# Kernel tuning notes

Measured on AMD Instinct MI355X. Metric: run time of the kernel, lower is better.

The kernel has to match this reference:

```python
import jax, jax.numpy as jnp
import numpy as np

N = 100000
E = 1600000
F_IN = 128
HID = 64
N_CLS = 16


def gcn_conv(x, row, col, W, b, n_nodes):
    # x: [N, Fin]; row/col: [E+N] (self-loops already appended)
    h = x @ W  # [N, Fout]
    ones = jnp.ones(row.shape[0], dtype=x.dtype)
    deg = jax.ops.segment_sum(ones, col, num_segments=n_nodes)  # in-degree incl. self-loop
    dinv = jnp.where(deg > 0, jax.lax.rsqrt(deg), 0.0)
    norm = dinv[row] * dinv[col]  # [E+N]
    msg = h[row] * norm[:, None]  # gather + scale
    out = jax.ops.segment_sum(msg, col, num_segments=n_nodes)  # scatter-add
    return out + b


def setup_inputs() -> dict:
    key = jax.random.key(0)
    k1, k2, k3, k4, k5, k6 = jax.random.split(key, 6)
    x = jax.random.normal(k1, (N, F_IN), dtype=jnp.float32)
    edge_index = jax.random.randint(k2, (2, E), 0, N, dtype=jnp.int64)
    # Glorot-ish init for weights
    W1 = jax.random.normal(k3, (F_IN, HID), dtype=jnp.float32) / np.sqrt(F_IN)
    b1 = jnp.zeros((HID,), dtype=jnp.float32)
    W2 = jax.random.normal(k4, (HID, N_CLS), dtype=jnp.float32) / np.sqrt(HID)
    b2 = jnp.zeros((N_CLS,), dtype=jnp.float32)
    return {"x": x, "edge_index": edge_index, "W1": W1, "b1": b1, "W2": W2, "b2": b2}


def reference(x, edge_index, W1, b1, W2, b2):
    # Add self-loops (GCNConv default add_self_loops=True)
    loop = jnp.arange(N, dtype=edge_index.dtype)
    row = jnp.concatenate([edge_index[0], loop])
    col = jnp.concatenate([edge_index[1], loop])
    h = gcn_conv(x, row, col, W1, b1, N)
    h = jax.nn.relu(h)
    h = gcn_conv(h, row, col, W2, b2, N)
    return jax.nn.log_softmax(h, axis=1)
```

## Files before the change

kernel.cpp:

```cpp
#include <hip/hip_runtime.h>
#include <hip/hip_fp16.h>

#define F_IN 128
#define HID  64
#define NCLS 16
#define NPB  128
#define CAP  4096
#define CHUNK 16384
#define W1PAD 136
#define CSTRIDE 4

typedef _Float16 half_t;
typedef __attribute__((ext_vector_type(8))) _Float16 half8;
typedef __attribute__((ext_vector_type(4))) float float4v;


__global__ __launch_bounds__(256) void bin_gemm(
    const int* __restrict__ row, const int* __restrict__ col,
    const float* __restrict__ x, const float* __restrict__ W1,
    int* __restrict__ cursor, int* __restrict__ ebuf,
    __half* __restrict__ hs1, int N, int E, int NB, int nbin)
{
    __shared__ __align__(16) char smem[17408];
    int t = threadIdx.x;

    if ((int)blockIdx.x < nbin) {
        int* hist = (int*)smem;
        int* base = (int*)smem + 1024;
        int* off  = (int*)smem + 2048;
        for (int i = t; i < NB; i += 256) hist[i] = 0;
        int base_e = blockIdx.x * CHUNK;
        __syncthreads();
        #pragma unroll 4
        for (int s = 0; s < 16; ++s) {
            int ej = base_e + s * 1024 + t * 4;
            int nv = min(max(E - ej, 0), 4);
            if (nv == 4) {
                int4 c4 = *(const int4*)&col[ej];
                atomicAdd(&hist[c4.x >> 7], 1);
                atomicAdd(&hist[c4.y >> 7], 1);
                atomicAdd(&hist[c4.z >> 7], 1);
                atomicAdd(&hist[c4.w >> 7], 1);
            } else {
                for (int q = ej; q < E; ++q) atomicAdd(&hist[col[q] >> 7], 1);
            }
        }
        __syncthreads();
        for (int i = t; i < NB; i += 256) {
            int h = hist[i];
            base[i] = h ? (i * CAP + atomicAdd(&cursor[i * CSTRIDE], h)) : 0;
            off[i] = 0;
        }
        __syncthreads();
        #pragma unroll 4
        for (int s = 0; s < 16; ++s) {
            int ej = base_e + s * 1024 + t * 4;
            int nv = min(max(E - ej, 0), 4);
            if (nv == 4) {
                int4 c4 = *(const int4*)&col[ej];
                int4 r4 = *(const int4*)&row[ej];
                int b0 = c4.x >> 7; int p0 = base[b0] + atomicAdd(&off[b0], 1);
                if (p0 < (b0 + 1) * CAP) ebuf[p0] = (r4.x << 7) | (c4.x & (NPB - 1));
                int b1 = c4.y >> 7; int p1 = base[b1] + atomicAdd(&off[b1], 1);
                if (p1 < (b1 + 1) * CAP) ebuf[p1] = (r4.y << 7) | (c4.y & (NPB - 1));
                int b2 = c4.z >> 7; int p2 = base[b2] + atomicAdd(&off[b2], 1);
                if (p2 < (b2 + 1) * CAP) ebuf[p2] = (r4.z << 7) | (c4.z & (NPB - 1));
                int b3 = c4.w >> 7; int p3 = base[b3] + atomicAdd(&off[b3], 1);
                if (p3 < (b3 + 1) * CAP) ebuf[p3] = (r4.w << 7) | (c4.w & (NPB - 1));
            } else {
                for (int q = ej; q < E; ++q) {
                    int c = col[q], b = c >> 7;
                    int p = base[b] + atomicAdd(&off[b], 1);
                    if (p < (b + 1) * CAP) ebuf[p] = (row[q] << 7) | (c & (NPB - 1));
                }
            }
        }
        return;
    }

    half_t* W1l = (half_t*)smem;
    for (int i = t; i < F_IN * HID; i += 256) {
        int k = i >> 6, n = i & 63;
        W1l[n * W1PAD + k] = (half_t)W1[i];
    }
    __syncthreads();

    int b = blockIdx.x - nbin;
    int node0 = b << 7;
    int wv = t >> 6, lane = t & 63;
    int l15 = lane & 15, quad = lane >> 4;
    int mbase = wv * 32;
    int r0 = min(node0 + mbase + l15, N - 1);
    int r1 = min(node0 + mbase + 16 + l15, N - 1);
    const float* x0 = x + (size_t)r0 * F_IN;
    const float* x1 = x + (size_t)r1 * F_IN;
    float4v acc[2][4];
    #pragma unroll
    for (int mt = 0; mt < 2; ++mt)
        #pragma unroll
        for (int j = 0; j < 4; ++j) acc[mt][j] = (float4v){0.f, 0.f, 0.f, 0.f};
    #pragma unroll
    for (int kb = 0; kb < 4; ++kb) {
        int off = kb * 32 + quad * 8;
        float4 fa = *(const float4*)&x0[off];
        float4 fb = *(const float4*)&x0[off + 4];
        float4 ga = *(const float4*)&x1[off];
        float4 gb = *(const float4*)&x1[off + 4];
        half8 a0 = {(half_t)fa.x, (half_t)fa.y, (half_t)fa.z, (half_t)fa.w,
                    (half_t)fb.x, (half_t)fb.y, (half_t)fb.z, (half_t)fb.w};
        half8 a1 = {(half_t)ga.x, (half_t)ga.y, (half_t)ga.z, (half_t)ga.w,
                    (half_t)gb.x, (half_t)gb.y, (half_t)gb.z, (half_t)gb.w};
        #pragma unroll
        for (int j = 0; j < 4; ++j) {
            half8 bv = *(const half8*)&W1l[(j * 16 + l15) * W1PAD + off];
            acc[0][j] = __builtin_amdgcn_mfma_f32_16x16x32_f16(a0, bv, acc[0][j], 0, 0, 0);
            acc[1][j] = __builtin_amdgcn_mfma_f32_16x16x32_f16(a1, bv, acc[1][j], 0, 0, 0);
        }
    }
    #pragma unroll
    for (int mt = 0; mt < 2; ++mt)
        #pragma unroll
        for (int j = 0; j < 4; ++j)
            #pragma unroll
            for (int r = 0; r < 4; ++r) {
                int m = mbase + mt * 16 + quad * 4 + r;
                int nn = node0 + m;
                if (nn < N) hs1[(size_t)nn * HID + j * 16 + l15] =
                    __float2half(acc[mt][j][r]);
            }
}


__global__ __launch_bounds__(256) void csr_scale(
    const int* __restrict__ ebuf, const int* __restrict__ cursor,
    int2* __restrict__ rsc, int* __restrict__ csr_row,
    __half* __restrict__ hs1, int N)
{
    __shared__ int hist[NPB];
    __shared__ float dv[NPB];
    __shared__ int cur[NPB];
    __shared__ int wtot;
    int t = threadIdx.x;
    int b = blockIdx.x;
    int node0 = b << 7;
    int ebase = b * CAP;

    int p[8];
    #pragma unroll
    for (int k = 0; k < 8; ++k) p[k] = ebuf[ebase + t + 256 * k];
    int cnt = min(cursor[b * CSTRIDE], CAP);
    if (t < NPB) hist[t] = 0;
    __syncthreads();
    #pragma unroll
    for (int k = 0; k < 8; ++k)
        if (t + 256 * k < cnt) atomicAdd(&hist[p[k] & (NPB - 1)], 1);
    if (cnt > 2048)
        for (int e = 2048 + t; e < cnt; e += 256)
            atomicAdd(&hist[ebuf[ebase + e] & (NPB - 1)], 1);
    __syncthreads();

    int h = 0, incl = 0;
    if (t < NPB) {
        h = hist[t];
        incl = h;
        #pragma unroll
        for (int off = 1; off < 64; off <<= 1) {
            int u = __shfl_up(incl, off, 64);
            if ((t & 63) >= off) incl += u;
        }
        if (t == 63) wtot = incl;
        dv[t] = rsqrtf((float)h + 1.0f);
    }
    __syncthreads();
    if (t < NPB) {
        if (t >= 64) incl += wtot;
        int start = ebase + incl - h;
        cur[t] = start;
        int n = node0 + t;
        if (n < N) rsc[n] = make_int2(start, h);
    }
    __syncthreads();

    #pragma unroll
    for (int k = 0; k < 8; ++k)
        if (t + 256 * k < cnt) {
            int pos = atomicAdd(&cur[p[k] & (NPB - 1)], 1);
            csr_row[pos] = p[k] >> 7;
        }
    if (cnt > 2048)
        for (int e = 2048 + t; e < cnt; e += 256) {
            int pp = ebuf[ebase + e];
            int pos = atomicAdd(&cur[pp & (NPB - 1)], 1);
            csr_row[pos] = pp >> 7;
        }

    half8* H = (half8*)hs1;
    for (int i = t; i < 1024; i += 256) {
        int r = i >> 3, s8 = i & 7;
        int n = node0 + r;
        if (n < N) {
            half8 v = H[(size_t)n * 8 + s8];
            float d = dv[r];
            #pragma unroll
            for (int k = 0; k < 8; ++k) v[k] = (half_t)((float)v[k] * d);
            H[(size_t)n * 8 + s8] = v;
        }
    }
}


__global__ __launch_bounds__(256) void agg_l1(
    const __half* __restrict__ hs1, const int2* __restrict__ rsc,
    const int* __restrict__ csr, const float* __restrict__ b1,
    const float* __restrict__ W2, __half* __restrict__ h2s, int N)
{
    __shared__ float W2l[HID * NCLS];
    __shared__ float o1[32][65];
    for (int i = threadIdx.x; i < HID * NCLS; i += 256) W2l[i] = W2[i];
    __syncthreads();
    int w = threadIdx.x >> 6, lane = threadIdx.x & 63;
    int g = lane >> 3, gl = lane & 7;
    int rowi = w * 8 + g;
    int c = blockIdx.x * 32 + rowi;
    bool active = (c < N);
    int cc = active ? c : 0;
    int2 rc = rsc[cc];
    int e0 = rc.x, e1 = rc.x + rc.y;
    float dc = rsqrtf((float)rc.y + 1.0f);
    const half8* H = (const half8*)hs1;
    half8 sv = H[(size_t)cc * 8 + gl];
    float sum[8];
    #pragma unroll
    for (int k = 0; k < 8; ++k) sum[k] = (float)sv[k];
    int i = e0;
    for (; i + 8 <= e1; i += 8) {
        int id[8];
        #pragma unroll
        for (int s = 0; s < 8; ++s) id[s] = csr[i + s];
        half8 a[8];
        #pragma unroll
        for (int s = 0; s < 8; ++s) a[s] = H[(size_t)id[s] * 8 + gl];
        half8 t0 = a[0] + a[1];
        half8 t1 = a[2] + a[3];
        half8 t2 = a[4] + a[5];
        half8 t3 = a[6] + a[7];
        half8 v = (t0 + t1) + (t2 + t3);
        #pragma unroll
        for (int k = 0; k < 8; ++k) sum[k] += (float)v[k];
    }
    if (i < e1) {
        int e1m1 = e1 - 1;
        int id[8];
        #pragma unroll
        for (int s = 0; s < 8; ++s) id[s] = csr[min(i + s, e1m1)];
        half8 a[8];
        #pragma unroll
        for (int s = 0; s < 8; ++s) a[s] = H[(size_t)id[s] * 8 + gl];
        #pragma unroll
        for (int s = 0; s < 8; ++s) {
            float fm = (i + s < e1) ? 1.f : 0.f;
            #pragma unroll
            for (int k = 0; k < 8; ++k) sum[k] = fmaf(fm, (float)a[s][k], sum[k]);
        }
    }
    float4 bb0 = *(const float4*)&b1[gl * 8];
    float4 bb1 = *(const float4*)&b1[gl * 8 + 4];
    o1[rowi][gl * 8 + 0] = fmaxf(fmaf(dc, sum[0], bb0.x), 0.f);
    o1[rowi][gl * 8 + 1] = fmaxf(fmaf(dc, sum[1], bb0.y), 0.f);
    o1[rowi][gl * 8 + 2] = fmaxf(fmaf(dc, sum[2], bb0.z), 0.f);
    o1[rowi][gl * 8 + 3] = fmaxf(fmaf(dc, sum[3], bb0.w), 0.f);
    o1[rowi][gl * 8 + 4] = fmaxf(fmaf(dc, sum[4], bb1.x), 0.f);
    o1[rowi][gl * 8 + 5] = fmaxf(fmaf(dc, sum[5], bb1.y), 0.f);
    o1[rowi][gl * 8 + 6] = fmaxf(fmaf(dc, sum[6], bb1.z), 0.f);
    o1[rowi][gl * 8 + 7] = fmaxf(fmaf(dc, sum[7], bb1.w), 0.f);
    int j0 = gl * 2, j1 = gl * 2 + 1;
    float s0 = 0.f, s1 = 0.f;
    const float* orow = o1[rowi];
    #pragma unroll 8
    for (int k = 0; k < HID; ++k) {
        float ov = orow[k];
        s0 = fmaf(ov, W2l[k * NCLS + j0], s0);
        s1 = fmaf(ov, W2l[k * NCLS + j1], s1);
    }
    if (active) {
        __half2 hv;
        hv.x = __float2half(dc * s0);
        hv.y = __float2half(dc * s1);
        ((__half2*)h2s)[(size_t)c * 8 + gl] = hv;
    }
}


__global__ __launch_bounds__(256) void agg2_final(
    const __half* __restrict__ h2s, const int2* __restrict__ rsc,
    const int* __restrict__ csr, const float* __restrict__ b2,
    float* __restrict__ out, int N)
{
    int t = threadIdx.x;
    int w = t >> 6, lane = t & 63;
    int nw = lane >> 1, hl = lane & 1;
    int c = blockIdx.x * 128 + w * 32 + nw;
    bool active = (c < N);
    int cc = active ? c : 0;
    int2 rc = rsc[cc];
    int e0 = rc.x, e1 = rc.x + rc.y;
    float dcv = rsqrtf((float)rc.y + 1.0f);
    const half8* H = (const half8*)h2s;
    half8 sv = H[(size_t)cc * 2 + hl];
    float sum[8];
    #pragma unroll
    for (int k = 0; k < 8; ++k) sum[k] = (float)sv[k];
    int i = e0;
    for (; i + 8 <= e1; i += 8) {
        int id[8];
        #pragma unroll
        for (int s = 0; s < 8; ++s) id[s] = csr[i + s];
        half8 a[8];
        #pragma unroll
        for (int s = 0; s < 8; ++s) a[s] = H[(size_t)id[s] * 2 + hl];
        half8 t0 = a[0] + a[1];
        half8 t1 = a[2] + a[3];
        half8 t2 = a[4] + a[5];
        half8 t3 = a[6] + a[7];
        half8 v = (t0 + t1) + (t2 + t3);
        #pragma unroll
        for (int k = 0; k < 8; ++k) sum[k] += (float)v[k];
    }
    if (i < e1) {
        int e1m1 = e1 - 1;
        int id[8];
        #pragma unroll
        for (int s = 0; s < 8; ++s) id[s] = csr[min(i + s, e1m1)];
        half8 a[8];
        #pragma unroll
        for (int s = 0; s < 8; ++s) a[s] = H[(size_t)id[s] * 2 + hl];
        #pragma unroll
        for (int s = 0; s < 8; ++s) {
            float fm = (i + s < e1) ? 1.f : 0.f;
            #pragma unroll
            for (int k = 0; k < 8; ++k) sum[k] = fmaf(fm, (float)a[s][k], sum[k]);
        }
    }
    float4 bb0 = *(const float4*)&b2[hl * 8];
    float4 bb1 = *(const float4*)&b2[hl * 8 + 4];
    float v0 = fmaf(dcv, sum[0], bb0.x);
    float v1 = fmaf(dcv, sum[1], bb0.y);
    float v2 = fmaf(dcv, sum[2], bb0.z);
    float v3 = fmaf(dcv, sum[3], bb0.w);
    float v4 = fmaf(dcv, sum[4], bb1.x);
    float v5 = fmaf(dcv, sum[5], bb1.y);
    float v6 = fmaf(dcv, sum[6], bb1.z);
    float v7 = fmaf(dcv, sum[7], bb1.w);
    float mx = fmaxf(fmaxf(fmaxf(v0, v1), fmaxf(v2, v3)),
                     fmaxf(fmaxf(v4, v5), fmaxf(v6, v7)));
    mx = fmaxf(mx, __shfl_xor(mx, 1, 64));
    float s = __expf(v0 - mx) + __expf(v1 - mx) + __expf(v2 - mx) + __expf(v3 - mx)
            + __expf(v4 - mx) + __expf(v5 - mx) + __expf(v6 - mx) + __expf(v7 - mx);
    s += __shfl_xor(s, 1, 64);
    float lse = mx + __logf(s);
    if (active) {
        float* o = out + (size_t)c * NCLS + hl * 8;
        *(float4*)&o[0] = make_float4(v0 - lse, v1 - lse, v2 - lse, v3 - lse);
        *(float4*)&o[4] = make_float4(v4 - lse, v5 - lse, v6 - lse, v7 - lse);
    }
}


extern "C" void kernel_launch(void* const* d_in, const int* in_sizes, int n_in,
                              void* d_out, int out_size, void* d_ws, size_t ws_size,
                              hipStream_t stream) {
    const float* x  = (const float*)d_in[0];
    const int*   ei = (const int*)d_in[1];
    const float* W1 = (const float*)d_in[2];
    const float* b1 = (const float*)d_in[3];
    const float* W2 = (const float*)d_in[4];
    const float* b2 = (const float*)d_in[5];
    float* out = (float*)d_out;

    const int N = in_sizes[0] / F_IN;
    const int E = in_sizes[1] / 2;
    const int* row = ei;
    const int* col = ei + E;

    const int NB = (N + NPB - 1) / NPB;
    size_t Np  = ((size_t)N + 15) & ~(size_t)15;
    size_t NBp = ((size_t)NB + 15) & ~(size_t)15;
    size_t Rg  = (size_t)NB * CAP;

    char* p = (char*)d_ws;
    __half* hs1     = (__half*)p;  p += Np * HID * 2;
    __half* h2s     = (__half*)p;  p += Np * NCLS * 2;
    int2*   rsc     = (int2*)p;    p += Np * 8;
    int*    csr_row = (int*)p;     p += Rg * 4;
    int*    ebuf    = (int*)p;     p += Rg * 4;
    int*    cursor  = (int*)p;     p += NBp * 4 * CSTRIDE;

    int nbin = (E + CHUNK - 1) / CHUNK;

    hipMemsetAsync(cursor, 0, NBp * sizeof(int) * CSTRIDE, stream);
    bin_gemm<<<nbin + NB, 256, 0, stream>>>(row, col, x, W1, cursor, ebuf,
                                            hs1, N, E, NB, nbin);
    csr_scale<<<NB, 256, 0, stream>>>(ebuf, cursor, rsc, csr_row, hs1, N);
    agg_l1<<<(N + 31) / 32, 256, 0, stream>>>(hs1, rsc, csr_row, b1, W2, h2s, N);
    agg2_final<<<(N + 127) / 128, 256, 0, stream>>>(h2s, rsc, csr_row, b2, out, N);
}
```

Measured before the change: 184.7 us.

## Split GEMM from binning and fuse dinv scaling into GEMM epilogue

The layer-1 GEMM moves out of the binning kernel into its own launch that runs after the CSR/degree kernel. This lets it multiply by dinv directly in the epilogue, which removes the separate read-modify-write pass over hs1 in csr_scale. Output goes through an LDS staging tile so rows are written as coalesced half8 stores. The W1 transpose is now done once into global memory and read from there instead of per-block LDS. The cost is one extra kernel launch and losing the overlap between binning and GEMM.

```diff
diff --git a/kernel.cpp b/kernel.cpp
--- a/kernel.cpp
+++ b/kernel.cpp
@@ -7,86 +7,161 @@
 #define NPB  128
 #define CAP  4096
 #define CHUNK 16384
-#define W1PAD 136
 #define CSTRIDE 4
+#define SPAD 72
 
 typedef _Float16 half_t;
 typedef __attribute__((ext_vector_type(8))) _Float16 half8;
 typedef __attribute__((ext_vector_type(4))) float float4v;
 
 
-__global__ __launch_bounds__(256) void bin_gemm(
+__global__ __launch_bounds__(256) void bin_w1(
     const int* __restrict__ row, const int* __restrict__ col,
-    const float* __restrict__ x, const float* __restrict__ W1,
-    int* __restrict__ cursor, int* __restrict__ ebuf,
-    __half* __restrict__ hs1, int N, int E, int NB, int nbin)
+    const float* __restrict__ W1, int* __restrict__ cursor,
+    int* __restrict__ ebuf, half_t* __restrict__ W1t,
+    int E, int NB, int nbin)
 {
-    __shared__ __align__(16) char smem[17408];
+    __shared__ int hist[1024], base[1024], off[1024];
     int t = threadIdx.x;
 
-    if ((int)blockIdx.x < nbin) {
-        int* hist = (int*)smem;
-        int* base = (int*)smem + 1024;
-        int* off  = (int*)smem + 2048;
-        for (int i = t; i < NB; i += 256) hist[i] = 0;
-        int base_e = blockIdx.x * CHUNK;
-        __syncthreads();
-        #pragma unroll 4
-        for (int s = 0; s < 16; ++s) {
-            int ej = base_e + s * 1024 + t * 4;
-            int nv = min(max(E - ej, 0), 4);
-            if (nv == 4) {
-                int4 c4 = *(const int4*)&col[ej];
-                atomicAdd(&hist[c4.x >> 7], 1);
-                atomicAdd(&hist[c4.y >> 7], 1);
-                atomicAdd(&hist[c4.z >> 7], 1);
-                atomicAdd(&hist[c4.w >> 7], 1);
-            } else {
-                for (int q = ej; q < E; ++q) atomicAdd(&hist[col[q] >> 7], 1);
+    if ((int)blockIdx.x >= nbin) {
+        for (int i = t; i < F_IN * HID; i += 256) {
+            int k = i >> 6, n = i & 63;
+            W1t[n * F_IN + k] = (half_t)W1[i];
+        }
+        return;
+    }
+    for (int i = t; i < NB; i += 256) hist[i] = 0;
+    int base_e = blockIdx.x * CHUNK;
+    __syncthreads();
+    #pragma unroll 4
+    for (int s = 0; s < 16; ++s) {
+        int ej = base_e + s * 1024 + t * 4;
+        int nv = min(max(E - ej, 0), 4);
+        if (nv == 4) {
+            int4 c4 = *(const int4*)&col[ej];
+            atomicAdd(&hist[c4.x >> 7], 1);
+            atomicAdd(&hist[c4.y >> 7], 1);
+            atomicAdd(&hist[c4.z >> 7], 1);
+            atomicAdd(&hist[c4.w >> 7], 1);
+        } else {
+            for (int q = ej; q < E; ++q) atomicAdd(&hist[col[q] >> 7], 1);
+        }
+    }
+    __syncthreads();
+    for (int i = t; i < NB; i += 256) {
+        int h = hist[i];
+        base[i] = h ? (i * CAP + atomicAdd(&cursor[i * CSTRIDE], h)) : 0;
+        off[i] = 0;
+    }
+    __syncthreads();
+    #pragma unroll 4
+    for (int s = 0; s < 16; ++s) {
+        int ej = base_e + s * 1024 + t * 4;
+        int nv = min(max(E - ej, 0), 4);
+        if (nv == 4) {
+            int4 c4 = *(const int4*)&col[ej];
+            int4 r4 = *(const int4*)&row[ej];
+            int b0 = c4.x >> 7; int p0 = base[b0] + atomicAdd(&off[b0], 1);
+            if (p0 < (b0 + 1) * CAP) ebuf[p0] = (r4.x << 7) | (c4.x & (NPB - 1));
+            int b1 = c4.y >> 7; int p1 = base[b1] + atomicAdd(&off[b1], 1);
+            if (p1 < (b1 + 1) * CAP) ebuf[p1] = (r4.y << 7) | (c4.y & (NPB - 1));
+            int b2 = c4.z >> 7; int p2 = base[b2] + atomicAdd(&off[b2], 1);
+            if (p2 < (b2 + 1) * CAP) ebuf[p2] = (r4.z << 7) | (c4.z & (NPB - 1));
+            int b3 = c4.w >> 7; int p3 = base[b3] + atomicAdd(&off[b3], 1);
+            if (p3 < (b3 + 1) * CAP) ebuf[p3] = (r4.w << 7) | (c4.w & (NPB - 1));
+        } else {
+            for (int q = ej; q < E; ++q) {
+                int c = col[q], b = c >> 7;
+                int p = base[b] + atomicAdd(&off[b], 1);
+                if (p < (b + 1) * CAP) ebuf[p] = (row[q] << 7) | (c & (NPB - 1));
             }
         }
-        __syncthreads();
-        for (int i = t; i < NB; i += 256) {
-            int h = hist[i];
-            base[i] = h ? (i * CAP + atomicAdd(&cursor[i * CSTRIDE], h)) : 0;
-            off[i] = 0;
-        }
-        __syncthreads();
-        #pragma unroll 4
-        for (int s = 0; s < 16; ++s) {
-            int ej = base_e + s * 1024 + t * 4;
-            int nv = min(max(E - ej, 0), 4);
-            if (nv == 4) {
-                int4 c4 = *(const int4*)&col[ej];
-                int4 r4 = *(const int4*)&row[ej];
-                int b0 = c4.x >> 7; int p0 = base[b0] + atomicAdd(&off[b0], 1);
-                if (p0 < (b0 + 1) * CAP) ebuf[p0] = (r4.x << 7) | (c4.x & (NPB - 1));
-                int b1 = c4.y >> 7; int p1 = base[b1] + atomicAdd(&off[b1], 1);
-                if (p1 < (b1 + 1) * CAP) ebuf[p1] = (r4.y << 7) | (c4.y & (NPB - 1));
-                int b2 = c4.z >> 7; int p2 = base[b2] + atomicAdd(&off[b2], 1);
-                if (p2 < (b2 + 1) * CAP) ebuf[p2] = (r4.z << 7) | (c4.z & (NPB - 1));
-                int b3 = c4.w >> 7; int p3 = base[b3] + atomicAdd(&off[b3], 1);
-                if (p3 < (b3 + 1) * CAP) ebuf[p3] = (r4.w << 7) | (c4.w & (NPB - 1));
-            } else {
-                for (int q = ej; q < E; ++q) {
-                    int c = col[q], b = c >> 7;
-                    int p = base[b] + atomicAdd(&off[b], 1);
-                    if (p < (b + 1) * CAP) ebuf[p] = (row[q] << 7) | (c & (NPB - 1));
-                }
-            }
-        }
-        return;
-    }
-
-    half_t* W1l = (half_t*)smem;
-    for (int i = t; i < F_IN * HID; i += 256) {
-        int k = i >> 6, n = i & 63;
-        W1l[n * W1PAD + k] = (half_t)W1[i];
-    }
-    __syncthreads();
-
-    int b = blockIdx.x - nbin;
+    }
+}
+
+
+__global__ __launch_bounds__(256) void csr_dinv(
+    const int* __restrict__ ebuf, const int* __restrict__ cursor,
+    int2* __restrict__ rsc, int* __restrict__ csr_row,
+    float* __restrict__ dinv, int N)
+{
+    __shared__ int hist[NPB];
+    __shared__ int cur[NPB];
+    __shared__ int wtot;
+    int t = threadIdx.x;
+    int b = blockIdx.x;
     int node0 = b << 7;
+    int ebase = b * CAP;
+
+    int p[8];
+    #pragma unroll
+    for (int k = 0; k < 8; ++k) p[k] = ebuf[ebase + t + 256 * k];
+    int cnt = min(cursor[b * CSTRIDE], CAP);
+    if (t < NPB) hist[t] = 0;
+    __syncthreads();
+    #pragma unroll
+    for (int k = 0; k < 8; ++k)
+        if (t + 256 * k < cnt) atomicAdd(&hist[p[k] & (NPB - 1)], 1);
+    if (cnt > 2048)
+        for (int e = 2048 + t; e < cnt; e += 256)
+            atomicAdd(&hist[ebuf[ebase + e] & (NPB - 1)], 1);
+    __syncthreads();
+
+    int h = 0, incl = 0;
+    if (t < NPB) {
+        h = hist[t];
+        incl = h;
+        #pragma unroll
+        for (int off = 1; off < 64; off <<= 1) {
+            int u = __shfl_up(incl, off, 64);
+            if ((t & 63) >= off) incl += u;
+        }
+        if (t == 63) wtot = incl;
+    }
+    __syncthreads();
+    if (t < NPB) {
+        if (t >= 64) incl += wtot;
+        int start = ebase + incl - h;
+        cur[t] = start;
+        int n = node0 + t;
+        if (n < N) {
+            rsc[n] = make_int2(start, h);
+            dinv[n] = rsqrtf((float)h + 1.0f);
+        }
+    }
+    __syncthreads();
+
+    #pragma unroll
+    for (int k = 0; k < 8; ++k)
+        if (t + 256 * k < cnt) {
+            int pos = atomicAdd(&cur[p[k] & (NPB - 1)], 1);
+            csr_row[pos] = p[k] >> 7;
+        }
+    if (cnt > 2048)
+        for (int e = 2048 + t; e < cnt; e += 256) {
+            int pp = ebuf[ebase + e];
+            int pos = atomicAdd(&cur[pp & (NPB - 1)], 1);
+            csr_row[pos] = pp >> 7;
+        }
+}
+
+
+__global__ __launch_bounds__(256) void gemm1(
+    const float* __restrict__ x, const half_t* __restrict__ W1t,
+    const float* __restrict__ dinv, __half* __restrict__ hs1, int N)
+{
+    __shared__ float dv[NPB];
+    __shared__ __align__(16) half_t stage[128 * SPAD];
+    int t = threadIdx.x;
+    int b = blockIdx.x;
+    int node0 = b << 7;
+    if (t < NPB) {
+        int n = node0 + t;
+        dv[t] = (n < N) ? dinv[n] : 0.f;
+    }
+    __syncthreads();
+
     int wv = t >> 6, lane = t & 63;
     int l15 = lane & 15, quad = lane >> 4;
     int mbase = wv * 32;
@@ -112,7 +187,7 @@
                     (half_t)gb.x, (half_t)gb.y, (half_t)gb.z, (half_t)gb.w};
         #pragma unroll
         for (int j = 0; j < 4; ++j) {
-            half8 bv = *(const half8*)&W1l[(j * 16 + l15) * W1PAD + off];
+            half8 bv = *(const half8*)&W1t[(size_t)(j * 16 + l15) * F_IN + off];
             acc[0][j] = __builtin_amdgcn_mfma_f32_16x16x32_f16(a0, bv, acc[0][j], 0, 0, 0);
             acc[1][j] = __builtin_amdgcn_mfma_f32_16x16x32_f16(a1, bv, acc[1][j], 0, 0, 0);
         }
@@ -124,87 +199,17 @@
             #pragma unroll
             for (int r = 0; r < 4; ++r) {
                 int m = mbase + mt * 16 + quad * 4 + r;
-                int nn = node0 + m;
-                if (nn < N) hs1[(size_t)nn * HID + j * 16 + l15] =
-                    __float2half(acc[mt][j][r]);
+                stage[m * SPAD + j * 16 + l15] = (half_t)(acc[mt][j][r] * dv[m]);
             }
-}
-
-
-__global__ __launch_bounds__(256) void csr_scale(
-    const int* __restrict__ ebuf, const int* __restrict__ cursor,
-    int2* __restrict__ rsc, int* __restrict__ csr_row,
-    __half* __restrict__ hs1, int N)
-{
-    __shared__ int hist[NPB];
-    __shared__ float dv[NPB];
-    __shared__ int cur[NPB];
-    __shared__ int wtot;
-    int t = threadIdx.x;
-    int b = blockIdx.x;
-    int node0 = b << 7;
-    int ebase = b * CAP;
-
-    int p[8];
-    #pragma unroll
-    for (int k = 0; k < 8; ++k) p[k] = ebuf[ebase + t + 256 * k];
-    int cnt = min(cursor[b * CSTRIDE], CAP);
-    if (t < NPB) hist[t] = 0;
-    __syncthreads();
-    #pragma unroll
-    for (int k = 0; k < 8; ++k)
-        if (t + 256 * k < cnt) atomicAdd(&hist[p[k] & (NPB - 1)], 1);
-    if (cnt > 2048)
-        for (int e = 2048 + t; e < cnt; e += 256)
-            atomicAdd(&hist[ebuf[ebase + e] & (NPB - 1)], 1);
-    __syncthreads();
-
-    int h = 0, incl = 0;
-    if (t < NPB) {
-        h = hist[t];
-        incl = h;
-        #pragma unroll
-        for (int off = 1; off < 64; off <<= 1) {
-            int u = __shfl_up(incl, off, 64);
-            if ((t & 63) >= off) incl += u;
-        }
-        if (t == 63) wtot = incl;
-        dv[t] = rsqrtf((float)h + 1.0f);
-    }
-    __syncthreads();
-    if (t < NPB) {
-        if (t >= 64) incl += wtot;
-        int start = ebase + incl - h;
-        cur[t] = start;
-        int n = node0 + t;
-        if (n < N) rsc[n] = make_int2(start, h);
-    }
-    __syncthreads();
-
-    #pragma unroll
-    for (int k = 0; k < 8; ++k)
-        if (t + 256 * k < cnt) {
-            int pos = atomicAdd(&cur[p[k] & (NPB - 1)], 1);
-            csr_row[pos] = p[k] >> 7;
-        }
-    if (cnt > 2048)
-        for (int e = 2048 + t; e < cnt; e += 256) {
-            int pp = ebuf[ebase + e];
-            int pos = atomicAdd(&cur[pp & (NPB - 1)], 1);
-            csr_row[pos] = pp >> 7;
-        }
-
-    half8* H = (half8*)hs1;
-    for (int i = t; i < 1024; i += 256) {
-        int r = i >> 3, s8 = i & 7;
-        int n = node0 + r;
-        if (n < N) {
-            half8 v = H[(size_t)n * 8 + s8];
-            float d = dv[r];
-            #pragma unroll
-            for (int k = 0; k < 8; ++k) v[k] = (half_t)((float)v[k] * d);
-            H[(size_t)n * 8 + s8] = v;
-        }
+    __syncthreads();
+    #pragma unroll
+    for (int k = 0; k < 4; ++k) {
+        int i = t + 256 * k;
+        int rrow = i >> 3, seg = i & 7;
+        int n = node0 + rrow;
+        if (n < N)
+            *(half8*)&((half_t*)hs1)[(size_t)n * HID + seg * 8] =
+                *(const half8*)&stage[rrow * SPAD + seg * 8];
     }
 }
 
@@ -390,6 +395,8 @@
     char* p = (char*)d_ws;
     __half* hs1     = (__half*)p;  p += Np * HID * 2;
     __half* h2s     = (__half*)p;  p += Np * NCLS * 2;
+    half_t* W1t     = (half_t*)p;  p += (size_t)F_IN * HID * 2;
+    float*  dinv    = (float*)p;   p += Np * 4;
     int2*   rsc     = (int2*)p;    p += Np * 8;
     int*    csr_row = (int*)p;     p += Rg * 4;
     int*    ebuf    = (int*)p;     p += Rg * 4;
@@ -398,9 +405,9 @@
     int nbin = (E + CHUNK - 1) / CHUNK;
 
     hipMemsetAsync(cursor, 0, NBp * sizeof(int) * CSTRIDE, stream);
-    bin_gemm<<<nbin + NB, 256, 0, stream>>>(row, col, x, W1, cursor, ebuf,
-                                            hs1, N, E, NB, nbin);
-    csr_scale<<<NB, 256, 0, stream>>>(ebuf, cursor, rsc, csr_row, hs1, N);
+    bin_w1<<<nbin + 1, 256, 0, stream>>>(row, col, W1, cursor, ebuf, W1t, E, NB, nbin);
+    csr_dinv<<<NB, 256, 0, stream>>>(ebuf, cursor, rsc, csr_row, dinv, N);
+    gemm1<<<NB, 256, 0, stream>>>(x, W1t, dinv, hs1, N);
     agg_l1<<<(N + 31) / 32, 256, 0, stream>>>(hs1, rsc, csr_row, b1, W2, h2s, N);
     agg2_final<<<(N + 127) / 128, 256, 0, stream>>>(h2s, rsc, csr_row, b2, out, N);
 }
```

New measurement: 193.2 us. 1.05x slower.
